# Optimization experiments

Measured on AMD Instinct MI355X. Metric: run time of the kernel, lower is better.

Reference implementation:

```python
import jax, jax.numpy as jnp
import numpy as np

MAX_LENGTH = 252
HID = 768
MLP = 770
NLAB = 36


def setup_inputs() -> dict:
    key = jax.random.key(0)
    ks = jax.random.split(key, 7)
    B = 2
    hidden = jax.random.normal(ks[0], (B, MAX_LENGTH + 1, HID), dtype=jnp.float32)
    pred_spans = jnp.sort(jax.random.randint(ks[1], (B, 2), 0, MAX_LENGTH), axis=1)
    span_mask = jax.random.randint(ks[2], (MAX_LENGTH, MAX_LENGTH), 0, 2).astype(jnp.int32)
    W1 = jax.random.normal(ks[3], (MLP, 2 * HID + 1), dtype=jnp.float32) * 0.02
    b1 = jax.random.normal(ks[4], (MLP,), dtype=jnp.float32) * 0.02
    W2 = jax.random.normal(ks[5], (NLAB, MLP), dtype=jnp.float32) * 0.02
    b2 = jax.random.normal(ks[6], (NLAB,), dtype=jnp.float32) * 0.02
    return {"hidden": hidden, "pred_spans": pred_spans, "span_mask": span_mask,
            "W1": W1, "b1": b1, "W2": W2, "b2": b2}


def reference(hidden, pred_spans, span_mask, W1, b1, W2, b2):
    L = MAX_LENGTH
    B = hidden.shape[0]
    vecs = hidden[:, 1:L + 1, :]                      # [B, L, 768] (skip [CLS])
    # Split concat-weight: feat = [vec_i, vec_j, indicator]
    W1i = W1[:, :HID]                                 # [770, 768]
    W1j = W1[:, HID:2 * HID]                          # [770, 768]
    w1c = W1[:, 2 * HID]                              # [770]
    Ai = jnp.einsum('bld,hd->blh', vecs, W1i)         # [B, L, 770]
    Aj = jnp.einsum('bld,hd->blh', vecs, W1j)         # [B, L, 770]
    # Predicate-span indicator: 2 if (i,j)==pred_span; 1 if strictly inside
    # combinations_with_replacement(start..end) minus (start,end); else 0.
    ii = jnp.arange(L)[:, None]
    jj = jnp.arange(L)[None, :]
    s = pred_spans[:, 0][:, None, None]
    e = pred_spans[:, 1][:, None, None]
    eq = (ii == s) & (jj == e)
    inside = (s <= ii) & (ii <= jj) & (jj <= e)
    ind = jnp.where(eq, 2.0, jnp.where(inside, 1.0, 0.0)).astype(hidden.dtype)  # [B,L,L]
    h = Ai[:, :, None, :] + Aj[:, None, :, :] + ind[..., None] * w1c + b1       # [B,L,L,770]
    h = jax.nn.relu(h)
    out = jnp.einsum('bijh,kh->bijk', h, W2) + b2     # [B, L, L, 36]
    valid = (span_mask >= 1)[None, :, :, None]
    out = jnp.where(valid, out, 0.0)                  # invalid pairs -> exact zeros
    out = out.reshape(B, L * L, NLAB)                 # pair dim = 63504
    res = jax.nn.log_softmax(out, axis=1)             # softmax over span pairs
    return jnp.transpose(res, (0, 2, 1))              # [B, 36, L*L]
```

## Files before the change

### kernel.cpp

```cpp
#include <hip/hip_runtime.h>
#include <hip/hip_bf16.h>
#include <math.h>

#define L 252
#define HID 768
#define MLP 770
#define NLAB 36
#define NB 2
#define M1 (NB*L)
#define N1 (2*MLP)
#define LL (L*L)
#define LL4 (LL/4)
#define KC 25
#define KC1 24
#define NT1P 100
#define NMT 32

typedef float f32x4 __attribute__((ext_vector_type(4)));
typedef short short8 __attribute__((ext_vector_type(8)));

#define AJF_OFF 0
#define AJF_FLOATS 204800
#define AIB_OFF (AJF_OFF + AJF_FLOATS)
#define AIB_FLOATS 604800
#define W2F_OFF (AIB_OFF + AIB_FLOATS)
#define W2F_FLOATS 19200
#define PART_OFF (W2F_OFF + W2F_FLOATS)
#define PART_FLOATS (72*1024*2)
#define W1F_OFF (PART_OFF + PART_FLOATS)
#define W1F_FLOATS (KC1*NT1P*64*4)
#define VBF_OFF (W1F_OFF + W1F_FLOATS)
#define VBF_FLOATS (NMT*KC1*64*4)
#define NW1F (KC1*NT1P*64)
#define NW2F (KC*3*64)
#define NVBF (NMT*KC1*64)

__device__ __forceinline__ void dma16(const void* g, void* l) {
  __builtin_amdgcn_global_load_lds(
      (const __attribute__((address_space(1))) unsigned int*)g,
      (__attribute__((address_space(3))) unsigned int*)l, 16, 0, 0);
}

__device__ __forceinline__ unsigned short bf16b(float x) {
  __hip_bfloat16 h = __float2bfloat16(x);
  return *reinterpret_cast<unsigned short*>(&h);
}

#define WAIT_VM0() __builtin_amdgcn_s_waitcnt(0x0F70)
#define WAIT_VM5() __builtin_amdgcn_s_waitcnt(0x0F75)

__global__ __launch_bounds__(256) void pack_kernel(const float* __restrict__ W1,
                                                   const float* __restrict__ W2,
                                                   const float* __restrict__ hid,
                                                   float* __restrict__ ws) {
  const int total = NW1F + NW2F + NVBF;
  int idx = blockIdx.x * 256 + threadIdx.x;
  if (idx >= total) return;
  if (idx < NW1F) {
    int kc = idx / (NT1P * 64);
    int rem = idx - kc * (NT1P * 64);
    int nt = rem / 64, lane = rem - nt * 64;
    int n = nt * 16 + (lane & 15);
    int kb = kc * 32 + (lane >> 4) * 8;
    unsigned int u[4];
#pragma unroll
    for (int p = 0; p < 4; p++) {
      unsigned short us[2];
#pragma unroll
      for (int q = 0; q < 2; q++) {
        int k = kb + 2 * p + q;
        float v = 0.f;
        if (n < N1) v = (n < MLP) ? W1[(size_t)n * 1537 + k]
                                  : W1[(size_t)(n - MLP) * 1537 + HID + k];
        us[q] = bf16b(v);
      }
      u[p] = (unsigned int)us[0] | ((unsigned int)us[1] << 16);
    }
    ((uint4*)(ws + W1F_OFF))[idx] = make_uint4(u[0], u[1], u[2], u[3]);
  } else if (idx < NW1F + NW2F) {
    int e2 = idx - NW1F;
    int kc = e2 / 192, rem = e2 - kc * 192;
    int tile = rem / 64, lane = rem - tile * 64;
    int label = tile * 16 + (lane & 15);
    int kb = kc * 32 + (lane >> 4) * 8;
    unsigned int u[4];
#pragma unroll
    for (int p = 0; p < 4; p++) {
      unsigned short us[2];
#pragma unroll
      for (int q = 0; q < 2; q++) {
        int k = kb + 2 * p + q;
        float v = (label < NLAB && k < MLP) ? W2[label * MLP + k] : 0.f;
        us[q] = bf16b(v);
      }
      u[p] = (unsigned int)us[0] | ((unsigned int)us[1] << 16);
    }
    ((uint4*)(ws + W2F_OFF))[e2] = make_uint4(u[0], u[1], u[2], u[3]);
  } else {
    int e3 = idx - NW1F - NW2F;
    int mt = e3 / (KC1 * 64);
    int rem = e3 - mt * (KC1 * 64);
    int kc = rem / 64, lane = rem - kc * 64;
    int m = mt * 16 + (lane & 15);
    int kb = kc * 32 + (lane >> 4) * 8;
    unsigned int u[4] = {0u, 0u, 0u, 0u};
    if (m < M1) {
      int b = (m >= L) ? 1 : 0;
      const float* src = hid + ((size_t)(b * (L + 1) + 1 + (m - b * L))) * HID + kb;
      float4 v0 = *(const float4*)src;
      float4 v1 = *(const float4*)(src + 4);
      float vv[8] = {v0.x, v0.y, v0.z, v0.w, v1.x, v1.y, v1.z, v1.w};
#pragma unroll
      for (int p = 0; p < 4; p++)
        u[p] = (unsigned int)bf16b(vv[2 * p]) | ((unsigned int)bf16b(vv[2 * p + 1]) << 16);
    }
    ((uint4*)(ws + VBF_OFF))[e3] = make_uint4(u[0], u[1], u[2], u[3]);
  }
}

__global__ __launch_bounds__(256, 2) void gemm1_kernel(const float* __restrict__ b1,
                                                       const float* __restrict__ W1,
                                                       const float* __restrict__ ws_ro,
                                                       unsigned short* __restrict__ AJF,
                                                       unsigned short* __restrict__ AiBh) {
  __shared__ char sm[61440];
  int t = threadIdx.x;
  int wave = t >> 6, lane = t & 63, lj = lane & 15, kh = lane >> 4;
  int nt0 = blockIdx.x * 4;
  int mt = blockIdx.y * 4 + wave;
  int m0 = mt * 16;
  const uint4* vbf = (const uint4*)(ws_ro + VBF_OFF) + (size_t)mt * KC1 * 64 + lane;
  const uint4* w1f = (const uint4*)(ws_ro + W1F_OFF);
  char* WB = sm + wave * 15360;
  char* bA = WB;
  char* bB = WB + 5120;
  char* bC = WB + 10240;

  f32x4 acc[4];
#pragma unroll
  for (int nt = 0; nt < 4; nt++) acc[nt] = (f32x4)(0.f);
  union FU { unsigned u[4]; short8 s8; };

  dma16(vbf, bA);
#pragma unroll
  for (int q = 0; q < 4; q++)
    dma16(&w1f[(size_t)(0 * NT1P + nt0 + q) * 64 + lane], bA + 1024 + q * 1024);
  dma16(vbf + 64, bB);
#pragma unroll
  for (int q = 0; q < 4; q++)
    dma16(&w1f[(size_t)(1 * NT1P + nt0 + q) * 64 + lane], bB + 1024 + q * 1024);

  for (int kc = 0; kc < KC1; kc++) {
    WAIT_VM5();
    uint4 av = *(const uint4*)(bA + lane * 16);
    uint4 bv[4];
#pragma unroll
    for (int q = 0; q < 4; q++) bv[q] = *(const uint4*)(bA + 1024 + q * 1024 + lane * 16);
    __builtin_amdgcn_sched_barrier(0);
    int kn = kc + 2; if (kn > KC1 - 1) kn = KC1 - 1;
    dma16(vbf + kn * 64, bC);
#pragma unroll
    for (int q = 0; q < 4; q++)
      dma16(&w1f[(size_t)(kn * NT1P + nt0 + q) * 64 + lane], bC + 1024 + q * 1024);
    __builtin_amdgcn_sched_barrier(0);
    { char* tmp = bA; bA = bB; bB = bC; bC = tmp; }
    FU af; af.u[0] = av.x; af.u[1] = av.y; af.u[2] = av.z; af.u[3] = av.w;
#pragma unroll
    for (int q = 0; q < 4; q++) {
      FU bf; bf.u[0] = bv[q].x; bf.u[1] = bv[q].y; bf.u[2] = bv[q].z; bf.u[3] = bv[q].w;
      acc[q] = __builtin_amdgcn_mfma_f32_16x16x32_bf16(af.s8, bf.s8, acc[q], 0, 0, 0);
    }
  }

#pragma unroll
  for (int nt = 0; nt < 4; nt++) {
    int nn = (nt0 + nt) * 16 + lj;
    if (nn >= N1) continue;
    if (nn < MLP) {
      float b1v = b1[nn];
      float wv = W1[(size_t)nn * 1537 + 1536];
#pragma unroll
      for (int r = 0; r < 4; r++) {
        int mm = m0 + kh * 4 + r;
        if (mm < M1) {
          float a = acc[nt][r] + b1v;
          AiBh[(size_t)(0 * M1 + mm) * 800 + nn] = bf16b(a);
          AiBh[(size_t)(1 * M1 + mm) * 800 + nn] = bf16b(a + wv);
          AiBh[(size_t)(2 * M1 + mm) * 800 + nn] = bf16b(a + 2.f * wv);
        }
      }
    } else {
      int hh = nn - MLP;
      int kcq = hh >> 5, kk = hh & 31;
      int l2hi = (kk >> 3) << 4, ee = kk & 7;
#pragma unroll
      for (int r = 0; r < 4; r++) {
        int mm = m0 + kh * 4 + r;
        if (mm < M1) {
          int bb2 = (mm >= L) ? 1 : 0;
          int jg = mm - bb2 * L;
          size_t rec = ((size_t)((bb2 * KC + kcq) * 16 + (jg >> 4)) * 64 + (l2hi | (jg & 15)));
          AJF[rec * 8 + ee] = bf16b(acc[nt][r]);
        }
      }
    }
  }
}

__global__ __launch_bounds__(256, 2) void main_kernel(
    const unsigned short* __restrict__ AJF,
    const unsigned short* __restrict__ AiBh,
    const uint4* __restrict__ wfr,
    const float* __restrict__ b2,
    const int* __restrict__ spans,
    const int* __restrict__ smask,
    float* __restrict__ out,
    float* __restrict__ part) {
  __shared__ char sm[61440];
  int t = threadIdx.x;
  int wave = t >> 6, lane = t & 63, lj = lane & 15, kh = lane >> 4;
  int j0 = blockIdx.x * 64;
  int i0 = blockIdx.y * 4;
  int b = blockIdx.z;
  int s = spans[2 * b], e = spans[2 * b + 1];
  int j = j0 + wave * 16 + lj;

  int poff[4];
#pragma unroll
  for (int ii = 0; ii < 4; ii++) {
    int i = i0 + ii;
    int ind = 0;
    if (i == s && j == e) ind = 2;
    else if (s <= i && i <= j && j <= e) ind = 1;
    poff[ii] = 1024 + ((ind * 4 + ii) * 4 + kh) * 16;
  }

  const unsigned short* aj_g = AJF + ((size_t)((b * KC + 0) * 16 + (j0 >> 4) + wave) * 64 + lane) * 8;
  int pr = lane >> 2; if (pr > 11) pr = 11;
  int pt = pr >> 2, pii = pr & 3, pc = lane & 3;
  const unsigned short* p_g = AiBh + (size_t)(pt * M1 + b * L + i0 + pii) * 800 + pc * 8;
  const uint4* wf_g = wfr + lane;
  char* WB = sm + wave * 15360;
  char* bA = WB;
  char* bB = WB + 5120;
  char* bC = WB + 10240;

  f32x4 acc[4][3];
#pragma unroll
  for (int ii = 0; ii < 4; ii++)
#pragma unroll
    for (int tl = 0; tl < 3; tl++) acc[ii][tl] = (f32x4)(0.f);
  union FU { unsigned u[4]; short8 s8; };

  dma16(aj_g, bA);
  dma16(p_g, bA + 1024);
  dma16(&wf_g[0 * 64], bA + 2048);
  dma16(&wf_g[1 * 64], bA + 3072);
  dma16(&wf_g[2 * 64], bA + 4096);
  dma16(aj_g + 8192, bB);
  dma16(p_g + 32, bB + 1024);
  dma16(&wf_g[3 * 64], bB + 2048);
  dma16(&wf_g[4 * 64], bB + 3072);
  dma16(&wf_g[5 * 64], bB + 4096);

  for (int kc = 0; kc < KC; kc++) {
    WAIT_VM5();
    uint4 av = *(const uint4*)(bA + lane * 16);
    uint4 w0 = *(const uint4*)(bA + 2048 + lane * 16);
    uint4 w1 = *(const uint4*)(bA + 3072 + lane * 16);
    uint4 w2v = *(const uint4*)(bA + 4096 + lane * 16);
    uint4 pv[4];
#pragma unroll
    for (int ii = 0; ii < 4; ii++) pv[ii] = *(const uint4*)(bA + poff[ii]);
    __builtin_amdgcn_sched_barrier(0);
    int kn = kc + 2; if (kn > KC - 1) kn = KC - 1;
    dma16(aj_g + (size_t)kn * 8192, bC);
    dma16(p_g + kn * 32, bC + 1024);
    dma16(&wf_g[(kn * 3 + 0) * 64], bC + 2048);
    dma16(&wf_g[(kn * 3 + 1) * 64], bC + 3072);
    dma16(&wf_g[(kn * 3 + 2) * 64], bC + 4096);
    __builtin_amdgcn_sched_barrier(0);
    { char* tmp = bA; bA = bB; bB = bC; bC = tmp; }
    float ajf[8];
    ajf[0] = __uint_as_float(av.x << 16); ajf[1] = __uint_as_float(av.x & 0xFFFF0000u);
    ajf[2] = __uint_as_float(av.y << 16); ajf[3] = __uint_as_float(av.y & 0xFFFF0000u);
    ajf[4] = __uint_as_float(av.z << 16); ajf[5] = __uint_as_float(av.z & 0xFFFF0000u);
    ajf[6] = __uint_as_float(av.w << 16); ajf[7] = __uint_as_float(av.w & 0xFFFF0000u);
    FU wf0, wf1, wf2;
    wf0.u[0] = w0.x; wf0.u[1] = w0.y; wf0.u[2] = w0.z; wf0.u[3] = w0.w;
    wf1.u[0] = w1.x; wf1.u[1] = w1.y; wf1.u[2] = w1.z; wf1.u[3] = w1.w;
    wf2.u[0] = w2v.x; wf2.u[1] = w2v.y; wf2.u[2] = w2v.z; wf2.u[3] = w2v.w;
#pragma unroll
    for (int ii = 0; ii < 4; ii++) {
      unsigned pu[4] = {pv[ii].x, pv[ii].y, pv[ii].z, pv[ii].w};
      FU fr;
#pragma unroll
      for (int q = 0; q < 4; q++) {
        float x0 = fmaxf(ajf[2 * q] + __uint_as_float(pu[q] << 16), 0.f);
        float x1 = fmaxf(ajf[2 * q + 1] + __uint_as_float(pu[q] & 0xFFFF0000u), 0.f);
        __hip_bfloat162 pk = __float22bfloat162_rn(make_float2(x0, x1));
        fr.u[q] = *reinterpret_cast<unsigned*>(&pk);
      }
      acc[ii][0] = __builtin_amdgcn_mfma_f32_16x16x32_bf16(fr.s8, wf0.s8, acc[ii][0], 0, 0, 0);
      acc[ii][1] = __builtin_amdgcn_mfma_f32_16x16x32_bf16(fr.s8, wf1.s8, acc[ii][1], 0, 0, 0);
      acc[ii][2] = __builtin_amdgcn_mfma_f32_16x16x32_bf16(fr.s8, wf2.s8, acc[ii][2], 0, 0, 0);
    }
  }

  float v[4][3][4];
#pragma unroll
  for (int ii = 0; ii < 4; ii++) {
    int i = i0 + ii;
    int smv[4];
#pragma unroll
    for (int r = 0; r < 4; r++) {
      int jr = j0 + wave * 16 + kh * 4 + r;
      smv[r] = (jr < L) ? smask[(size_t)i * L + jr] : 0;
    }
#pragma unroll
    for (int tl = 0; tl < 3; tl++) {
      int label = tl * 16 + lj;
      bool lab_ok = label < NLAB;
      float bbv = lab_ok ? b2[label] : 0.f;
#pragma unroll
      for (int r = 0; r < 4; r++) {
        int jr = j0 + wave * 16 + kh * 4 + r;
        float vv = -1e30f;
        if (jr < L && lab_ok) {
          vv = (smv[r] >= 1) ? acc[ii][tl][r] + bbv : 0.f;
          out[(size_t)(b * NLAB + label) * LL + (size_t)i * L + jr] = vv;
        }
        v[ii][tl][r] = vv;
      }
    }
  }
#pragma unroll
  for (int tl = 0; tl < 3; tl++) {
    float mx = -1e30f;
#pragma unroll
    for (int ii = 0; ii < 4; ii++)
#pragma unroll
      for (int r = 0; r < 4; r++) mx = fmaxf(mx, v[ii][tl][r]);
    mx = fmaxf(mx, __shfl_xor(mx, 16, 64));
    mx = fmaxf(mx, __shfl_xor(mx, 32, 64));
    float ssum = 0.f;
#pragma unroll
    for (int ii = 0; ii < 4; ii++)
#pragma unroll
      for (int r = 0; r < 4; r++) {
        float vv = v[ii][tl][r];
        ssum += (vv > -1e29f) ? __expf(vv - mx) : 0.f;
      }
    ssum += __shfl_xor(ssum, 16, 64);
    ssum += __shfl_xor(ssum, 32, 64);
    int label = tl * 16 + lj;
    if (kh == 0 && label < NLAB) {
      int slot = (blockIdx.x * 63 + blockIdx.y) * 4 + wave;
      float2* pp = (float2*)part + (size_t)(b * NLAB + label) * 1024 + slot;
      *pp = make_float2(mx, ssum);
    }
  }
}

__global__ __launch_bounds__(256) void finish_kernel(const float* __restrict__ part,
                                                     float* __restrict__ out) {
  int bk = blockIdx.y, cx = blockIdx.x;
  int t = threadIdx.x, wave = t >> 6, lane = t & 63;
  const float2* pp = (const float2*)part + (size_t)bk * 1024;
  float m = -1e30f, ss = 0.f;
  for (int idx = t; idx < 1008; idx += 256) {
    float2 q = pp[idx];
    if (q.x > m) { ss = ss * __expf(m - q.x) + q.y; m = q.x; }
    else ss += q.y * __expf(q.x - m);
  }
#pragma unroll
  for (int o = 1; o < 64; o <<= 1) {
    float m2 = __shfl_xor(m, o, 64);
    float s2 = __shfl_xor(ss, o, 64);
    if (m2 > m) { ss = ss * __expf(m - m2) + s2; m = m2; }
    else ss += s2 * __expf(m2 - m);
  }
  __shared__ float rm[4], rs[4], lsh;
  if (lane == 0) { rm[wave] = m; rs[wave] = ss; }
  __syncthreads();
  if (t == 0) {
    float M = rm[0], S = rs[0];
#pragma unroll
    for (int w = 1; w < 4; w++) {
      float m2 = rm[w], s2 = rs[w];
      if (m2 > M) { S = S * __expf(M - m2) + s2; M = m2; }
      else S += s2 * __expf(m2 - M);
    }
    lsh = M + logf(S);
  }
  __syncthreads();
  float l = lsh;
  float4* po = (float4*)(out + (size_t)bk * LL);
  int start = cx * 1985;
  int end = start + 1985; if (end > LL4) end = LL4;
  for (int idx = start + t; idx < end; idx += 256) {
    float4 v = po[idx];
    v.x -= l; v.y -= l; v.z -= l; v.w -= l;
    po[idx] = v;
  }
}

extern "C" void kernel_launch(void* const* d_in, const int* in_sizes, int n_in,
                              void* d_out, int out_size, void* d_ws, size_t ws_size,
                              hipStream_t stream) {
  const float* hidden = (const float*)d_in[0];
  const int* spans    = (const int*)d_in[1];
  const int* smask    = (const int*)d_in[2];
  const float* W1     = (const float*)d_in[3];
  const float* b1     = (const float*)d_in[4];
  const float* W2     = (const float*)d_in[5];
  const float* b2     = (const float*)d_in[6];
  float* ws = (float*)d_ws;
  unsigned short* AJF  = (unsigned short*)(ws + AJF_OFF);
  unsigned short* AiBh = (unsigned short*)(ws + AIB_OFF);
  const uint4* wfr     = (const uint4*)(ws + W2F_OFF);
  float* part          = ws + PART_OFF;
  float* out = (float*)d_out;

  const int total_pack = NW1F + NW2F + NVBF;
  pack_kernel<<<(total_pack + 255) / 256, 256, 0, stream>>>(W1, W2, hidden, ws);
  gemm1_kernel<<<dim3(25, 8), 256, 0, stream>>>(b1, W1, ws, AJF, AiBh);
  main_kernel<<<dim3(4, 63, NB), 256, 0, stream>>>(AJF, AiBh, wfr, b2, spans, smask, out, part);
  finish_kernel<<<dim3(8, NB * NLAB), 256, 0, stream>>>(part, out);
}
```

Before: 137.1 us.

## Fuse four kernels into one cooperative persistent kernel with grid syncs

Merges the pack, first GEMM, main pair-MLP, and log-softmax finish kernels into a single cooperative launch of 504 blocks, separating stages with grid.sync(). This removes three kernel launches and the gaps between them. In exchange it adds grid-wide barrier costs, leaves some blocks idle during the GEMM stage, and requires all 504 blocks to be co-resident (two per CU under the launch bounds).

```diff
diff --git a/kernel.cpp b/kernel.cpp
--- a/kernel.cpp
+++ b/kernel.cpp
@@ -1,6 +1,9 @@
 #include <hip/hip_runtime.h>
 #include <hip/hip_bf16.h>
+#include <hip/hip_cooperative_groups.h>
 #include <math.h>
+
+namespace cg = cooperative_groups;
 
 #define L 252
 #define HID 768
@@ -15,6 +18,7 @@
 #define KC1 24
 #define NT1P 100
 #define NMT 32
+#define GRID 504
 
 typedef float f32x4 __attribute__((ext_vector_type(4)));
 typedef short short8 __attribute__((ext_vector_type(8)));
@@ -49,359 +53,367 @@
 #define WAIT_VM0() __builtin_amdgcn_s_waitcnt(0x0F70)
 #define WAIT_VM5() __builtin_amdgcn_s_waitcnt(0x0F75)
 
-__global__ __launch_bounds__(256) void pack_kernel(const float* __restrict__ W1,
-                                                   const float* __restrict__ W2,
-                                                   const float* __restrict__ hid,
-                                                   float* __restrict__ ws) {
-  const int total = NW1F + NW2F + NVBF;
-  int idx = blockIdx.x * 256 + threadIdx.x;
-  if (idx >= total) return;
-  if (idx < NW1F) {
-    int kc = idx / (NT1P * 64);
-    int rem = idx - kc * (NT1P * 64);
-    int nt = rem / 64, lane = rem - nt * 64;
-    int n = nt * 16 + (lane & 15);
-    int kb = kc * 32 + (lane >> 4) * 8;
-    unsigned int u[4];
-#pragma unroll
-    for (int p = 0; p < 4; p++) {
-      unsigned short us[2];
-#pragma unroll
-      for (int q = 0; q < 2; q++) {
-        int k = kb + 2 * p + q;
-        float v = 0.f;
-        if (n < N1) v = (n < MLP) ? W1[(size_t)n * 1537 + k]
-                                  : W1[(size_t)(n - MLP) * 1537 + HID + k];
-        us[q] = bf16b(v);
-      }
-      u[p] = (unsigned int)us[0] | ((unsigned int)us[1] << 16);
-    }
-    ((uint4*)(ws + W1F_OFF))[idx] = make_uint4(u[0], u[1], u[2], u[3]);
-  } else if (idx < NW1F + NW2F) {
-    int e2 = idx - NW1F;
-    int kc = e2 / 192, rem = e2 - kc * 192;
-    int tile = rem / 64, lane = rem - tile * 64;
-    int label = tile * 16 + (lane & 15);
-    int kb = kc * 32 + (lane >> 4) * 8;
-    unsigned int u[4];
-#pragma unroll
-    for (int p = 0; p < 4; p++) {
-      unsigned short us[2];
-#pragma unroll
-      for (int q = 0; q < 2; q++) {
-        int k = kb + 2 * p + q;
-        float v = (label < NLAB && k < MLP) ? W2[label * MLP + k] : 0.f;
-        us[q] = bf16b(v);
-      }
-      u[p] = (unsigned int)us[0] | ((unsigned int)us[1] << 16);
-    }
-    ((uint4*)(ws + W2F_OFF))[e2] = make_uint4(u[0], u[1], u[2], u[3]);
-  } else {
-    int e3 = idx - NW1F - NW2F;
-    int mt = e3 / (KC1 * 64);
-    int rem = e3 - mt * (KC1 * 64);
-    int kc = rem / 64, lane = rem - kc * 64;
-    int m = mt * 16 + (lane & 15);
-    int kb = kc * 32 + (lane >> 4) * 8;
-    unsigned int u[4] = {0u, 0u, 0u, 0u};
-    if (m < M1) {
-      int b = (m >= L) ? 1 : 0;
-      const float* src = hid + ((size_t)(b * (L + 1) + 1 + (m - b * L))) * HID + kb;
-      float4 v0 = *(const float4*)src;
-      float4 v1 = *(const float4*)(src + 4);
-      float vv[8] = {v0.x, v0.y, v0.z, v0.w, v1.x, v1.y, v1.z, v1.w};
-#pragma unroll
-      for (int p = 0; p < 4; p++)
-        u[p] = (unsigned int)bf16b(vv[2 * p]) | ((unsigned int)bf16b(vv[2 * p + 1]) << 16);
-    }
-    ((uint4*)(ws + VBF_OFF))[e3] = make_uint4(u[0], u[1], u[2], u[3]);
-  }
-}
-
-__global__ __launch_bounds__(256, 2) void gemm1_kernel(const float* __restrict__ b1,
-                                                       const float* __restrict__ W1,
-                                                       const float* __restrict__ ws_ro,
-                                                       unsigned short* __restrict__ AJF,
-                                                       unsigned short* __restrict__ AiBh) {
+__global__ __launch_bounds__(256, 2) void mega_kernel(
+    const float* __restrict__ hid, const int* __restrict__ spans,
+    const int* __restrict__ smask, const float* __restrict__ W1,
+    const float* __restrict__ b1, const float* __restrict__ W2,
+    const float* __restrict__ b2, float* __restrict__ ws,
+    float* __restrict__ out) {
+  cg::grid_group grid = cg::this_grid();
   __shared__ char sm[61440];
   int t = threadIdx.x;
+  int blk = blockIdx.x;
   int wave = t >> 6, lane = t & 63, lj = lane & 15, kh = lane >> 4;
-  int nt0 = blockIdx.x * 4;
-  int mt = blockIdx.y * 4 + wave;
-  int m0 = mt * 16;
-  const uint4* vbf = (const uint4*)(ws_ro + VBF_OFF) + (size_t)mt * KC1 * 64 + lane;
-  const uint4* w1f = (const uint4*)(ws_ro + W1F_OFF);
-  char* WB = sm + wave * 15360;
-  char* bA = WB;
-  char* bB = WB + 5120;
-  char* bC = WB + 10240;
-
-  f32x4 acc[4];
-#pragma unroll
-  for (int nt = 0; nt < 4; nt++) acc[nt] = (f32x4)(0.f);
-  union FU { unsigned u[4]; short8 s8; };
-
-  dma16(vbf, bA);
-#pragma unroll
-  for (int q = 0; q < 4; q++)
-    dma16(&w1f[(size_t)(0 * NT1P + nt0 + q) * 64 + lane], bA + 1024 + q * 1024);
-  dma16(vbf + 64, bB);
-#pragma unroll
-  for (int q = 0; q < 4; q++)
-    dma16(&w1f[(size_t)(1 * NT1P + nt0 + q) * 64 + lane], bB + 1024 + q * 1024);
-
-  for (int kc = 0; kc < KC1; kc++) {
-    WAIT_VM5();
-    uint4 av = *(const uint4*)(bA + lane * 16);
-    uint4 bv[4];
-#pragma unroll
-    for (int q = 0; q < 4; q++) bv[q] = *(const uint4*)(bA + 1024 + q * 1024 + lane * 16);
-    __builtin_amdgcn_sched_barrier(0);
-    int kn = kc + 2; if (kn > KC1 - 1) kn = KC1 - 1;
-    dma16(vbf + kn * 64, bC);
+
+  unsigned short* AJF  = (unsigned short*)(ws + AJF_OFF);
+  unsigned short* AiBh = (unsigned short*)(ws + AIB_OFF);
+  uint4* W2F           = (uint4*)(ws + W2F_OFF);
+  float* part          = ws + PART_OFF;
+
+  {
+    const int total = NW1F + NW2F + NVBF;
+    for (int idx = blk * 256 + t; idx < total; idx += GRID * 256) {
+      if (idx < NW1F) {
+        int kc = idx / (NT1P * 64);
+        int rem = idx - kc * (NT1P * 64);
+        int nt = rem / 64, ln = rem - nt * 64;
+        int n = nt * 16 + (ln & 15);
+        int kb = kc * 32 + (ln >> 4) * 8;
+        unsigned int u[4];
+#pragma unroll
+        for (int p = 0; p < 4; p++) {
+          unsigned short us[2];
+#pragma unroll
+          for (int q = 0; q < 2; q++) {
+            int k = kb + 2 * p + q;
+            float v = 0.f;
+            if (n < N1) v = (n < MLP) ? W1[(size_t)n * 1537 + k]
+                                      : W1[(size_t)(n - MLP) * 1537 + HID + k];
+            us[q] = bf16b(v);
+          }
+          u[p] = (unsigned int)us[0] | ((unsigned int)us[1] << 16);
+        }
+        ((uint4*)(ws + W1F_OFF))[idx] = make_uint4(u[0], u[1], u[2], u[3]);
+      } else if (idx < NW1F + NW2F) {
+        int e2 = idx - NW1F;
+        int kc = e2 / 192, rem = e2 - kc * 192;
+        int tile = rem / 64, ln = rem - tile * 64;
+        int label = tile * 16 + (ln & 15);
+        int kb = kc * 32 + (ln >> 4) * 8;
+        unsigned int u[4];
+#pragma unroll
+        for (int p = 0; p < 4; p++) {
+          unsigned short us[2];
+#pragma unroll
+          for (int q = 0; q < 2; q++) {
+            int k = kb + 2 * p + q;
+            float v = (label < NLAB && k < MLP) ? W2[label * MLP + k] : 0.f;
+            us[q] = bf16b(v);
+          }
+          u[p] = (unsigned int)us[0] | ((unsigned int)us[1] << 16);
+        }
+        W2F[e2] = make_uint4(u[0], u[1], u[2], u[3]);
+      } else {
+        int e3 = idx - NW1F - NW2F;
+        int mt = e3 / (KC1 * 64);
+        int rem = e3 - mt * (KC1 * 64);
+        int kc = rem / 64, ln = rem - kc * 64;
+        int m = mt * 16 + (ln & 15);
+        int kb = kc * 32 + (ln >> 4) * 8;
+        unsigned int u[4] = {0u, 0u, 0u, 0u};
+        if (m < M1) {
+          int b = (m >= L) ? 1 : 0;
+          const float* src = hid + ((size_t)(b * (L + 1) + 1 + (m - b * L))) * HID + kb;
+          float4 v0 = *(const float4*)src;
+          float4 v1 = *(const float4*)(src + 4);
+          float vv[8] = {v0.x, v0.y, v0.z, v0.w, v1.x, v1.y, v1.z, v1.w};
+#pragma unroll
+          for (int p = 0; p < 4; p++)
+            u[p] = (unsigned int)bf16b(vv[2 * p]) | ((unsigned int)bf16b(vv[2 * p + 1]) << 16);
+        }
+        ((uint4*)(ws + VBF_OFF))[e3] = make_uint4(u[0], u[1], u[2], u[3]);
+      }
+    }
+  }
+  grid.sync();
+
+  if (blk < 200) {
+    int gx = blk % 25, gy = blk / 25;
+    int nt0 = gx * 4;
+    int mt = gy * 4 + wave;
+    int m0 = mt * 16;
+    const uint4* vbf = (const uint4*)(ws + VBF_OFF) + (size_t)mt * KC1 * 64 + lane;
+    const uint4* w1f = (const uint4*)(ws + W1F_OFF);
+    char* WB = sm + wave * 15360;
+    char* bA = WB;
+    char* bB = WB + 5120;
+    char* bC = WB + 10240;
+
+    f32x4 acc[4];
+#pragma unroll
+    for (int nt = 0; nt < 4; nt++) acc[nt] = (f32x4)(0.f);
+    union FU { unsigned u[4]; short8 s8; };
+
+    dma16(vbf, bA);
 #pragma unroll
     for (int q = 0; q < 4; q++)
-      dma16(&w1f[(size_t)(kn * NT1P + nt0 + q) * 64 + lane], bC + 1024 + q * 1024);
-    __builtin_amdgcn_sched_barrier(0);
-    { char* tmp = bA; bA = bB; bB = bC; bC = tmp; }
-    FU af; af.u[0] = av.x; af.u[1] = av.y; af.u[2] = av.z; af.u[3] = av.w;
-#pragma unroll
-    for (int q = 0; q < 4; q++) {
-      FU bf; bf.u[0] = bv[q].x; bf.u[1] = bv[q].y; bf.u[2] = bv[q].z; bf.u[3] = bv[q].w;
-      acc[q] = __builtin_amdgcn_mfma_f32_16x16x32_bf16(af.s8, bf.s8, acc[q], 0, 0, 0);
+      dma16(&w1f[(size_t)(0 * NT1P + nt0 + q) * 64 + lane], bA + 1024 + q * 1024);
+    dma16(vbf + 64, bB);
+#pragma unroll
+    for (int q = 0; q < 4; q++)
+      dma16(&w1f[(size_t)(1 * NT1P + nt0 + q) * 64 + lane], bB + 1024 + q * 1024);
+
+    for (int kc = 0; kc < KC1; kc++) {
+      WAIT_VM5();
+      uint4 av = *(const uint4*)(bA + lane * 16);
+      uint4 bv[4];
+#pragma unroll
+      for (int q = 0; q < 4; q++) bv[q] = *(const uint4*)(bA + 1024 + q * 1024 + lane * 16);
+      __builtin_amdgcn_sched_barrier(0);
+      int kn = kc + 2; if (kn > KC1 - 1) kn = KC1 - 1;
+      dma16(vbf + kn * 64, bC);
+#pragma unroll
+      for (int q = 0; q < 4; q++)
+        dma16(&w1f[(size_t)(kn * NT1P + nt0 + q) * 64 + lane], bC + 1024 + q * 1024);
+      __builtin_amdgcn_sched_barrier(0);
+      { char* tmp = bA; bA = bB; bB = bC; bC = tmp; }
+      FU af; af.u[0] = av.x; af.u[1] = av.y; af.u[2] = av.z; af.u[3] = av.w;
+#pragma unroll
+      for (int q = 0; q < 4; q++) {
+        FU bf; bf.u[0] = bv[q].x; bf.u[1] = bv[q].y; bf.u[2] = bv[q].z; bf.u[3] = bv[q].w;
+        acc[q] = __builtin_amdgcn_mfma_f32_16x16x32_bf16(af.s8, bf.s8, acc[q], 0, 0, 0);
+      }
+    }
+    WAIT_VM0();
+
+#pragma unroll
+    for (int nt = 0; nt < 4; nt++) {
+      int nn = (nt0 + nt) * 16 + lj;
+      if (nn >= N1) continue;
+      if (nn < MLP) {
+        float b1v = b1[nn];
+        float wv = W1[(size_t)nn * 1537 + 1536];
+#pragma unroll
+        for (int r = 0; r < 4; r++) {
+          int mm = m0 + kh * 4 + r;
+          if (mm < M1) {
+            float a = acc[nt][r] + b1v;
+            AiBh[(size_t)(0 * M1 + mm) * 800 + nn] = bf16b(a);
+            AiBh[(size_t)(1 * M1 + mm) * 800 + nn] = bf16b(a + wv);
+            AiBh[(size_t)(2 * M1 + mm) * 800 + nn] = bf16b(a + 2.f * wv);
+          }
+        }
+      } else {
+        int hh = nn - MLP;
+        int kcq = hh >> 5, kk = hh & 31;
+        int l2hi = (kk >> 3) << 4, ee = kk & 7;
+#pragma unroll
+        for (int r = 0; r < 4; r++) {
+          int mm = m0 + kh * 4 + r;
+          if (mm < M1) {
+            int bb2 = (mm >= L) ? 1 : 0;
+            int jg = mm - bb2 * L;
+            size_t rec = ((size_t)((bb2 * KC + kcq) * 16 + (jg >> 4)) * 64 + (l2hi | (jg & 15)));
+            AJF[rec * 8 + ee] = bf16b(acc[nt][r]);
+          }
+        }
+      }
     }
   }
-
-#pragma unroll
-  for (int nt = 0; nt < 4; nt++) {
-    int nn = (nt0 + nt) * 16 + lj;
-    if (nn >= N1) continue;
-    if (nn < MLP) {
-      float b1v = b1[nn];
-      float wv = W1[(size_t)nn * 1537 + 1536];
-#pragma unroll
-      for (int r = 0; r < 4; r++) {
-        int mm = m0 + kh * 4 + r;
-        if (mm < M1) {
-          float a = acc[nt][r] + b1v;
-          AiBh[(size_t)(0 * M1 + mm) * 800 + nn] = bf16b(a);
-          AiBh[(size_t)(1 * M1 + mm) * 800 + nn] = bf16b(a + wv);
-          AiBh[(size_t)(2 * M1 + mm) * 800 + nn] = bf16b(a + 2.f * wv);
-        }
-      }
-    } else {
-      int hh = nn - MLP;
-      int kcq = hh >> 5, kk = hh & 31;
-      int l2hi = (kk >> 3) << 4, ee = kk & 7;
-#pragma unroll
-      for (int r = 0; r < 4; r++) {
-        int mm = m0 + kh * 4 + r;
-        if (mm < M1) {
-          int bb2 = (mm >= L) ? 1 : 0;
-          int jg = mm - bb2 * L;
-          size_t rec = ((size_t)((bb2 * KC + kcq) * 16 + (jg >> 4)) * 64 + (l2hi | (jg & 15)));
-          AJF[rec * 8 + ee] = bf16b(acc[nt][r]);
-        }
-      }
-    }
-  }
-}
-
-__global__ __launch_bounds__(256, 2) void main_kernel(
-    const unsigned short* __restrict__ AJF,
-    const unsigned short* __restrict__ AiBh,
-    const uint4* __restrict__ wfr,
-    const float* __restrict__ b2,
-    const int* __restrict__ spans,
-    const int* __restrict__ smask,
-    float* __restrict__ out,
-    float* __restrict__ part) {
-  __shared__ char sm[61440];
-  int t = threadIdx.x;
-  int wave = t >> 6, lane = t & 63, lj = lane & 15, kh = lane >> 4;
-  int j0 = blockIdx.x * 64;
-  int i0 = blockIdx.y * 4;
-  int b = blockIdx.z;
-  int s = spans[2 * b], e = spans[2 * b + 1];
-  int j = j0 + wave * 16 + lj;
-
-  int poff[4];
-#pragma unroll
-  for (int ii = 0; ii < 4; ii++) {
-    int i = i0 + ii;
-    int ind = 0;
-    if (i == s && j == e) ind = 2;
-    else if (s <= i && i <= j && j <= e) ind = 1;
-    poff[ii] = 1024 + ((ind * 4 + ii) * 4 + kh) * 16;
-  }
-
-  const unsigned short* aj_g = AJF + ((size_t)((b * KC + 0) * 16 + (j0 >> 4) + wave) * 64 + lane) * 8;
-  int pr = lane >> 2; if (pr > 11) pr = 11;
-  int pt = pr >> 2, pii = pr & 3, pc = lane & 3;
-  const unsigned short* p_g = AiBh + (size_t)(pt * M1 + b * L + i0 + pii) * 800 + pc * 8;
-  const uint4* wf_g = wfr + lane;
-  char* WB = sm + wave * 15360;
-  char* bA = WB;
-  char* bB = WB + 5120;
-  char* bC = WB + 10240;
-
-  f32x4 acc[4][3];
-#pragma unroll
-  for (int ii = 0; ii < 4; ii++)
-#pragma unroll
-    for (int tl = 0; tl < 3; tl++) acc[ii][tl] = (f32x4)(0.f);
-  union FU { unsigned u[4]; short8 s8; };
-
-  dma16(aj_g, bA);
-  dma16(p_g, bA + 1024);
-  dma16(&wf_g[0 * 64], bA + 2048);
-  dma16(&wf_g[1 * 64], bA + 3072);
-  dma16(&wf_g[2 * 64], bA + 4096);
-  dma16(aj_g + 8192, bB);
-  dma16(p_g + 32, bB + 1024);
-  dma16(&wf_g[3 * 64], bB + 2048);
-  dma16(&wf_g[4 * 64], bB + 3072);
-  dma16(&wf_g[5 * 64], bB + 4096);
-
-  for (int kc = 0; kc < KC; kc++) {
-    WAIT_VM5();
-    uint4 av = *(const uint4*)(bA + lane * 16);
-    uint4 w0 = *(const uint4*)(bA + 2048 + lane * 16);
-    uint4 w1 = *(const uint4*)(bA + 3072 + lane * 16);
-    uint4 w2v = *(const uint4*)(bA + 4096 + lane * 16);
-    uint4 pv[4];
-#pragma unroll
-    for (int ii = 0; ii < 4; ii++) pv[ii] = *(const uint4*)(bA + poff[ii]);
-    __builtin_amdgcn_sched_barrier(0);
-    int kn = kc + 2; if (kn > KC - 1) kn = KC - 1;
-    dma16(aj_g + (size_t)kn * 8192, bC);
-    dma16(p_g + kn * 32, bC + 1024);
-    dma16(&wf_g[(kn * 3 + 0) * 64], bC + 2048);
-    dma16(&wf_g[(kn * 3 + 1) * 64], bC + 3072);
-    dma16(&wf_g[(kn * 3 + 2) * 64], bC + 4096);
-    __builtin_amdgcn_sched_barrier(0);
-    { char* tmp = bA; bA = bB; bB = bC; bC = tmp; }
-    float ajf[8];
-    ajf[0] = __uint_as_float(av.x << 16); ajf[1] = __uint_as_float(av.x & 0xFFFF0000u);
-    ajf[2] = __uint_as_float(av.y << 16); ajf[3] = __uint_as_float(av.y & 0xFFFF0000u);
-    ajf[4] = __uint_as_float(av.z << 16); ajf[5] = __uint_as_float(av.z & 0xFFFF0000u);
-    ajf[6] = __uint_as_float(av.w << 16); ajf[7] = __uint_as_float(av.w & 0xFFFF0000u);
-    FU wf0, wf1, wf2;
-    wf0.u[0] = w0.x; wf0.u[1] = w0.y; wf0.u[2] = w0.z; wf0.u[3] = w0.w;
-    wf1.u[0] = w1.x; wf1.u[1] = w1.y; wf1.u[2] = w1.z; wf1.u[3] = w1.w;
-    wf2.u[0] = w2v.x; wf2.u[1] = w2v.y; wf2.u[2] = w2v.z; wf2.u[3] = w2v.w;
+  grid.sync();
+
+  {
+    int mx_ = blk & 3;
+    int my_ = (blk >> 2) % 63;
+    int b = blk / 252;
+    int j0 = mx_ * 64;
+    int i0 = my_ * 4;
+    int s = spans[2 * b], e = spans[2 * b + 1];
+    int j = j0 + wave * 16 + lj;
+
+    int poff[4];
 #pragma unroll
     for (int ii = 0; ii < 4; ii++) {
-      unsigned pu[4] = {pv[ii].x, pv[ii].y, pv[ii].z, pv[ii].w};
-      FU fr;
-#pragma unroll
-      for (int q = 0; q < 4; q++) {
-        float x0 = fmaxf(ajf[2 * q] + __uint_as_float(pu[q] << 16), 0.f);
-        float x1 = fmaxf(ajf[2 * q + 1] + __uint_as_float(pu[q] & 0xFFFF0000u), 0.f);
-        __hip_bfloat162 pk = __float22bfloat162_rn(make_float2(x0, x1));
-        fr.u[q] = *reinterpret_cast<unsigned*>(&pk);
-      }
-      acc[ii][0] = __builtin_amdgcn_mfma_f32_16x16x32_bf16(fr.s8, wf0.s8, acc[ii][0], 0, 0, 0);
-      acc[ii][1] = __builtin_amdgcn_mfma_f32_16x16x32_bf16(fr.s8, wf1.s8, acc[ii][1], 0, 0, 0);
-      acc[ii][2] = __builtin_amdgcn_mfma_f32_16x16x32_bf16(fr.s8, wf2.s8, acc[ii][2], 0, 0, 0);
-    }
-  }
-
-  float v[4][3][4];
-#pragma unroll
-  for (int ii = 0; ii < 4; ii++) {
-    int i = i0 + ii;
-    int smv[4];
-#pragma unroll
-    for (int r = 0; r < 4; r++) {
-      int jr = j0 + wave * 16 + kh * 4 + r;
-      smv[r] = (jr < L) ? smask[(size_t)i * L + jr] : 0;
-    }
-#pragma unroll
-    for (int tl = 0; tl < 3; tl++) {
-      int label = tl * 16 + lj;
-      bool lab_ok = label < NLAB;
-      float bbv = lab_ok ? b2[label] : 0.f;
+      int i = i0 + ii;
+      int ind = 0;
+      if (i == s && j == e) ind = 2;
+      else if (s <= i && i <= j && j <= e) ind = 1;
+      poff[ii] = 1024 + ((ind * 4 + ii) * 4 + kh) * 16;
+    }
+
+    const unsigned short* aj_g = AJF + ((size_t)((b * KC + 0) * 16 + (j0 >> 4) + wave) * 64 + lane) * 8;
+    int pr = lane >> 2; if (pr > 11) pr = 11;
+    int pt = pr >> 2, pii = pr & 3, pc = lane & 3;
+    const unsigned short* p_g = AiBh + (size_t)(pt * M1 + b * L + i0 + pii) * 800 + pc * 8;
+    const uint4* wf_g = (const uint4*)W2F + lane;
+    char* WB = sm + wave * 15360;
+    char* bA = WB;
+    char* bB = WB + 5120;
+    char* bC = WB + 10240;
+
+    f32x4 acc[4][3];
+#pragma unroll
+    for (int ii = 0; ii < 4; ii++)
+#pragma unroll
+      for (int tl = 0; tl < 3; tl++) acc[ii][tl] = (f32x4)(0.f);
+    union FU { unsigned u[4]; short8 s8; };
+
+    dma16(aj_g, bA);
+    dma16(p_g, bA + 1024);
+    dma16(&wf_g[0 * 64], bA + 2048);
+    dma16(&wf_g[1 * 64], bA + 3072);
+    dma16(&wf_g[2 * 64], bA + 4096);
+    dma16(aj_g + 8192, bB);
+    dma16(p_g + 32, bB + 1024);
+    dma16(&wf_g[3 * 64], bB + 2048);
+    dma16(&wf_g[4 * 64], bB + 3072);
+    dma16(&wf_g[5 * 64], bB + 4096);
+
+    for (int kc = 0; kc < KC; kc++) {
+      WAIT_VM5();
+      uint4 av = *(const uint4*)(bA + lane * 16);
+      uint4 w0 = *(const uint4*)(bA + 2048 + lane * 16);
+      uint4 w1 = *(const uint4*)(bA + 3072 + lane * 16);
+      uint4 w2v = *(const uint4*)(bA + 4096 + lane * 16);
+      uint4 pv[4];
+#pragma unroll
+      for (int ii = 0; ii < 4; ii++) pv[ii] = *(const uint4*)(bA + poff[ii]);
+      __builtin_amdgcn_sched_barrier(0);
+      int kn = kc + 2; if (kn > KC - 1) kn = KC - 1;
+      dma16(aj_g + (size_t)kn * 8192, bC);
+      dma16(p_g + kn * 32, bC + 1024);
+      dma16(&wf_g[(kn * 3 + 0) * 64], bC + 2048);
+      dma16(&wf_g[(kn * 3 + 1) * 64], bC + 3072);
+      dma16(&wf_g[(kn * 3 + 2) * 64], bC + 4096);
+      __builtin_amdgcn_sched_barrier(0);
+      { char* tmp = bA; bA = bB; bB = bC; bC = tmp; }
+      float ajf[8];
+      ajf[0] = __uint_as_float(av.x << 16); ajf[1] = __uint_as_float(av.x & 0xFFFF0000u);
+      ajf[2] = __uint_as_float(av.y << 16); ajf[3] = __uint_as_float(av.y & 0xFFFF0000u);
+      ajf[4] = __uint_as_float(av.z << 16); ajf[5] = __uint_as_float(av.z & 0xFFFF0000u);
+      ajf[6] = __uint_as_float(av.w << 16); ajf[7] = __uint_as_float(av.w & 0xFFFF0000u);
+      FU wf0, wf1, wf2;
+      wf0.u[0] = w0.x; wf0.u[1] = w0.y; wf0.u[2] = w0.z; wf0.u[3] = w0.w;
+      wf1.u[0] = w1.x; wf1.u[1] = w1.y; wf1.u[2] = w1.z; wf1.u[3] = w1.w;
+      wf2.u[0] = w2v.x; wf2.u[1] = w2v.y; wf2.u[2] = w2v.z; wf2.u[3] = w2v.w;
+#pragma unroll
+      for (int ii = 0; ii < 4; ii++) {
+        unsigned pu[4] = {pv[ii].x, pv[ii].y, pv[ii].z, pv[ii].w};
+        FU fr;
+#pragma unroll
+        for (int q = 0; q < 4; q++) {
+          float x0 = fmaxf(ajf[2 * q] + __uint_as_float(pu[q] << 16), 0.f);
+          float x1 = fmaxf(ajf[2 * q + 1] + __uint_as_float(pu[q] & 0xFFFF0000u), 0.f);
+          __hip_bfloat162 pk = __float22bfloat162_rn(make_float2(x0, x1));
+          fr.u[q] = *reinterpret_cast<unsigned*>(&pk);
+        }
+        acc[ii][0] = __builtin_amdgcn_mfma_f32_16x16x32_bf16(fr.s8, wf0.s8, acc[ii][0], 0, 0, 0);
+        acc[ii][1] = __builtin_amdgcn_mfma_f32_16x16x32_bf16(fr.s8, wf1.s8, acc[ii][1], 0, 0, 0);
+        acc[ii][2] = __builtin_amdgcn_mfma_f32_16x16x32_bf16(fr.s8, wf2.s8, acc[ii][2], 0, 0, 0);
+      }
+    }
+    WAIT_VM0();
+
+    float v[4][3][4];
+#pragma unroll
+    for (int ii = 0; ii < 4; ii++) {
+      int i = i0 + ii;
+      int smv[4];
 #pragma unroll
       for (int r = 0; r < 4; r++) {
         int jr = j0 + wave * 16 + kh * 4 + r;
-        float vv = -1e30f;
-        if (jr < L && lab_ok) {
-          vv = (smv[r] >= 1) ? acc[ii][tl][r] + bbv : 0.f;
-          out[(size_t)(b * NLAB + label) * LL + (size_t)i * L + jr] = vv;
-        }
-        v[ii][tl][r] = vv;
+        smv[r] = (jr < L) ? smask[(size_t)i * L + jr] : 0;
+      }
+#pragma unroll
+      for (int tl = 0; tl < 3; tl++) {
+        int label = tl * 16 + lj;
+        bool lab_ok = label < NLAB;
+        float bbv = lab_ok ? b2[label] : 0.f;
+#pragma unroll
+        for (int r = 0; r < 4; r++) {
+          int jr = j0 + wave * 16 + kh * 4 + r;
+          float vv = -1e30f;
+          if (jr < L && lab_ok) {
+            vv = (smv[r] >= 1) ? acc[ii][tl][r] + bbv : 0.f;
+            out[(size_t)(b * NLAB + label) * LL + (size_t)i * L + jr] = vv;
+          }
+          v[ii][tl][r] = vv;
+        }
+      }
+    }
+#pragma unroll
+    for (int tl = 0; tl < 3; tl++) {
+      float mx = -1e30f;
+#pragma unroll
+      for (int ii = 0; ii < 4; ii++)
+#pragma unroll
+        for (int r = 0; r < 4; r++) mx = fmaxf(mx, v[ii][tl][r]);
+      mx = fmaxf(mx, __shfl_xor(mx, 16, 64));
+      mx = fmaxf(mx, __shfl_xor(mx, 32, 64));
+      float ssum = 0.f;
+#pragma unroll
+      for (int ii = 0; ii < 4; ii++)
+#pragma unroll
+        for (int r = 0; r < 4; r++) {
+          float vv = v[ii][tl][r];
+          ssum += (vv > -1e29f) ? __expf(vv - mx) : 0.f;
+        }
+      ssum += __shfl_xor(ssum, 16, 64);
+      ssum += __shfl_xor(ssum, 32, 64);
+      int label = tl * 16 + lj;
+      if (kh == 0 && label < NLAB) {
+        int slot = (mx_ * 63 + my_) * 4 + wave;
+        float2* pp = (float2*)part + (size_t)(b * NLAB + label) * 1024 + slot;
+        *pp = make_float2(mx, ssum);
       }
     }
   }
-#pragma unroll
-  for (int tl = 0; tl < 3; tl++) {
-    float mx = -1e30f;
-#pragma unroll
-    for (int ii = 0; ii < 4; ii++)
-#pragma unroll
-      for (int r = 0; r < 4; r++) mx = fmaxf(mx, v[ii][tl][r]);
-    mx = fmaxf(mx, __shfl_xor(mx, 16, 64));
-    mx = fmaxf(mx, __shfl_xor(mx, 32, 64));
-    float ssum = 0.f;
-#pragma unroll
-    for (int ii = 0; ii < 4; ii++)
-#pragma unroll
-      for (int r = 0; r < 4; r++) {
-        float vv = v[ii][tl][r];
-        ssum += (vv > -1e29f) ? __expf(vv - mx) : 0.f;
-      }
-    ssum += __shfl_xor(ssum, 16, 64);
-    ssum += __shfl_xor(ssum, 32, 64);
-    int label = tl * 16 + lj;
-    if (kh == 0 && label < NLAB) {
-      int slot = (blockIdx.x * 63 + blockIdx.y) * 4 + wave;
-      float2* pp = (float2*)part + (size_t)(b * NLAB + label) * 1024 + slot;
-      *pp = make_float2(mx, ssum);
-    }
-  }
-}
-
-__global__ __launch_bounds__(256) void finish_kernel(const float* __restrict__ part,
-                                                     float* __restrict__ out) {
-  int bk = blockIdx.y, cx = blockIdx.x;
-  int t = threadIdx.x, wave = t >> 6, lane = t & 63;
-  const float2* pp = (const float2*)part + (size_t)bk * 1024;
-  float m = -1e30f, ss = 0.f;
-  for (int idx = t; idx < 1008; idx += 256) {
-    float2 q = pp[idx];
-    if (q.x > m) { ss = ss * __expf(m - q.x) + q.y; m = q.x; }
-    else ss += q.y * __expf(q.x - m);
-  }
-#pragma unroll
-  for (int o = 1; o < 64; o <<= 1) {
-    float m2 = __shfl_xor(m, o, 64);
-    float s2 = __shfl_xor(ss, o, 64);
-    if (m2 > m) { ss = ss * __expf(m - m2) + s2; m = m2; }
-    else ss += s2 * __expf(m2 - m);
-  }
-  __shared__ float rm[4], rs[4], lsh;
-  if (lane == 0) { rm[wave] = m; rs[wave] = ss; }
-  __syncthreads();
-  if (t == 0) {
-    float M = rm[0], S = rs[0];
-#pragma unroll
-    for (int w = 1; w < 4; w++) {
-      float m2 = rm[w], s2 = rs[w];
-      if (m2 > M) { S = S * __expf(M - m2) + s2; M = m2; }
-      else S += s2 * __expf(m2 - M);
-    }
-    lsh = M + logf(S);
-  }
-  __syncthreads();
-  float l = lsh;
-  float4* po = (float4*)(out + (size_t)bk * LL);
-  int start = cx * 1985;
-  int end = start + 1985; if (end > LL4) end = LL4;
-  for (int idx = start + t; idx < end; idx += 256) {
-    float4 v = po[idx];
-    v.x -= l; v.y -= l; v.z -= l; v.w -= l;
-    po[idx] = v;
+  grid.sync();
+
+  {
+    float* rm = (float*)sm;
+    float* rs = rm + 4;
+    float* lshp = rs + 4;
+    for (int u = blk; u < 576; u += GRID) {
+      int cx = u & 7, bk = u >> 3;
+      const float2* pp = (const float2*)part + (size_t)bk * 1024;
+      float m = -1e30f, ss = 0.f;
+      for (int idx = t; idx < 1008; idx += 256) {
+        float2 q = pp[idx];
+        if (q.x > m) { ss = ss * __expf(m - q.x) + q.y; m = q.x; }
+        else ss += q.y * __expf(q.x - m);
+      }
+#pragma unroll
+      for (int o = 1; o < 64; o <<= 1) {
+        float m2 = __shfl_xor(m, o, 64);
+        float s2 = __shfl_xor(ss, o, 64);
+        if (m2 > m) { ss = ss * __expf(m - m2) + s2; m = m2; }
+        else ss += s2 * __expf(m2 - m);
+      }
+      if (lane == 0) { rm[wave] = m; rs[wave] = ss; }
+      __syncthreads();
+      if (t == 0) {
+        float M = rm[0], S = rs[0];
+#pragma unroll
+        for (int w = 1; w < 4; w++) {
+          float m2 = rm[w], s2 = rs[w];
+          if (m2 > M) { S = S * __expf(M - m2) + s2; M = m2; }
+          else S += s2 * __expf(m2 - M);
+        }
+        *lshp = M + logf(S);
+      }
+      __syncthreads();
+      float l = *lshp;
+      float4* po = (float4*)(out + (size_t)bk * LL);
+      int start = cx * 1985;
+      int end = start + 1985; if (end > LL4) end = LL4;
+      for (int idx = start + t; idx < end; idx += 256) {
+        float4 vv = po[idx];
+        vv.x -= l; vv.y -= l; vv.z -= l; vv.w -= l;
+        po[idx] = vv;
+      }
+      __syncthreads();
+    }
   }
 }
 
@@ -415,16 +427,10 @@
   const float* b1     = (const float*)d_in[4];
   const float* W2     = (const float*)d_in[5];
   const float* b2     = (const float*)d_in[6];
-  float* ws = (float*)d_ws;
-  unsigned short* AJF  = (unsigned short*)(ws + AJF_OFF);
-  unsigned short* AiBh = (unsigned short*)(ws + AIB_OFF);
-  const uint4* wfr     = (const uint4*)(ws + W2F_OFF);
-  float* part          = ws + PART_OFF;
+  float* ws  = (float*)d_ws;
   float* out = (float*)d_out;
 
-  const int total_pack = NW1F + NW2F + NVBF;
-  pack_kernel<<<(total_pack + 255) / 256, 256, 0, stream>>>(W1, W2, hidden, ws);
-  gemm1_kernel<<<dim3(25, 8), 256, 0, stream>>>(b1, W1, ws, AJF, AiBh);
-  main_kernel<<<dim3(4, 63, NB), 256, 0, stream>>>(AJF, AiBh, wfr, b2, spans, smask, out, part);
-  finish_kernel<<<dim3(8, NB * NLAB), 256, 0, stream>>>(part, out);
+  void* args[9] = {(void*)&hidden, (void*)&spans, (void*)&smask, (void*)&W1,
+                   (void*)&b1, (void*)&W2, (void*)&b2, (void*)&ws, (void*)&out};
+  hipLaunchCooperativeKernel((void*)mega_kernel, dim3(GRID), dim3(256), args, 0, stream);
 }
```

New measurement: 332.8 us. 2.43x slower.
